# Kernel optimization log

Hardware: AMD Instinct MI355X
Metric: run time of the kernel (lower is better)

The kernel has to match this reference:

```python
import math
import jax, jax.numpy as jnp
import numpy as np


def setup_inputs() -> dict:
    key = jax.random.key(0)
    k1, k2 = jax.random.split(key)
    B, Sq, Sk, H, Hkv, D = 2, 2048, 2048, 32, 8, 128
    q = jax.random.normal(k1, (B, Sq, H, D), dtype=jnp.float32)
    kv = jax.random.normal(k2, (B, Sk, 2, Hkv, D), dtype=jnp.float32)
    return {"q": q, "kv": kv}


def reference(q, kv):
    # q: [B, Sq, H, D]; kv: [B, Sk, 2, Hkv, D]
    H = q.shape[2]
    Hkv = kv.shape[3]
    if Hkv != H:
        # GQA: '... hkv d -> ... (hkv g) d' == repeat each kv head g times consecutively
        kv = jnp.repeat(kv, H // Hkv, axis=3)
    k = kv[:, :, 0]  # [B, Sk, H, D]
    v = kv[:, :, 1]  # [B, Sk, H, D]
    softmax_scale = 1.0 / math.sqrt(q.shape[-1])
    scores = jnp.einsum('bthd,bshd->bhts', q, k * softmax_scale)  # [B, H, Sq, Sk]
    attention = jax.nn.softmax(scores, axis=-1)
    # dropout p=0.0 -> identity
    output = jnp.einsum('bhts,bshd->bthd', attention, v)  # [B, Sq, H, D]
    return output
```

## Files before the change

### kernel.cpp

```cpp
#include <hip/hip_runtime.h>
#include <hip/hip_bf16.h>

typedef __attribute__((ext_vector_type(8))) short bf8_t;
typedef __attribute__((ext_vector_type(16))) float f32x16;

#ifndef __has_builtin
#define __has_builtin(x) 0
#endif
#if __has_builtin(__builtin_amdgcn_exp2f)
#define EXP2F(x) __builtin_amdgcn_exp2f(x)
#else
#define EXP2F(x) exp2f(x)
#endif

#define B_ 2
#define SQ_ 2048
#define SK_ 2048
#define H_ 32
#define HKV_ 8
#define D_ 128
#define KVSTRIDE (2 * HKV_ * D_)
#define QSTRIDE (H_ * D_)
#define NT (SK_ / 64)
#define SCLOG (0.08838834764831845f * 1.4426950408889634f)

__device__ __forceinline__ unsigned short f2bf(float f) {
  unsigned int u = __builtin_bit_cast(unsigned int, f);
  u += 0x7fffu + ((u >> 16) & 1u);
  return (unsigned short)(u >> 16);
}
__device__ __forceinline__ unsigned int pk2(float a, float b) {
  return (unsigned int)f2bf(a) | ((unsigned int)f2bf(b) << 16);
}

__global__ void __launch_bounds__(512, 2)
fattn2(const float* __restrict__ q, const float* __restrict__ kv,
       float* __restrict__ out) {
  __shared__ __align__(16) char lds[32768];
  char* Ksh = lds;
  char* Vsh = lds + 16384;

  const int tid = threadIdx.x;
  const int lane = tid & 63;
  const int w = tid >> 6;
  const int ql = lane & 31;
  const int hi = lane >> 5;

  const int bid = blockIdx.x;
  const int qt = bid & 7;
  const int h = (bid >> 3) & 31;
  const int b = bid >> 8;
  const int hkv = h >> 2;

  const float* qbase = q + ((size_t)b * SQ_ * H_ + h) * D_;
  const float* kbase = kv + ((size_t)b * SK_ * 2 * HKV_ + hkv) * D_;
  const float* vbase = kv + ((size_t)b * SK_ * 2 * HKV_ + HKV_ + hkv) * D_;

  const int qrow = qt * 256 + w * 32 + ql;
  const float* qp = qbase + (size_t)qrow * QSTRIDE;
  bf8_t qf[8];
#pragma unroll
  for (int step = 0; step < 8; ++step) {
    const int d0 = step * 16 + hi * 8;
    float4 a = *(const float4*)(qp + d0);
    float4 c = *(const float4*)(qp + d0 + 4);
    bf8_t tq;
    tq[0] = (short)f2bf(a.x * SCLOG); tq[1] = (short)f2bf(a.y * SCLOG);
    tq[2] = (short)f2bf(a.z * SCLOG); tq[3] = (short)f2bf(a.w * SCLOG);
    tq[4] = (short)f2bf(c.x * SCLOG); tq[5] = (short)f2bf(c.y * SCLOG);
    tq[6] = (short)f2bf(c.z * SCLOG); tq[7] = (short)f2bf(c.w * SCLOG);
    qf[step] = tq;
  }

  const int vkv = lane;
  int kcol;
  {
    const int wv = vkv & 31, bb = vkv >> 5;
    const int T_ = (wv >> 2) & 1;
    const int rr = (wv & 3) + ((wv >> 3) << 2);
    kcol = (((bb << 1) + (rr >> 3)) << 4) + (T_ << 3) + (rr & 7);
  }

  f32x16 o[4];
  f32x16 st[2];
#pragma unroll
  for (int i = 0; i < 4; ++i)
#pragma unroll
    for (int r = 0; r < 16; ++r) o[i][r] = 0.f;
  float m = -INFINITY, l = 0.f;

  float4 krg[4], vrg[4];
  const int krow0 = tid >> 5;
  const int kc4 = tid & 31;
  auto load_tiles = [&](int T) {
    const float* kp0 = kbase + ((size_t)T * 64 + krow0) * KVSTRIDE + kc4 * 4;
#pragma unroll
    for (int i = 0; i < 4; ++i)
      krg[i] = *(const float4*)(kp0 + (size_t)(16 * i) * KVSTRIDE);
    const float* vp0 = vbase + ((size_t)T * 64 + vkv) * KVSTRIDE + w * 16;
#pragma unroll
    for (int i = 0; i < 4; ++i) vrg[i] = *(const float4*)(vp0 + 4 * i);
  };
  load_tiles(0);

  for (int t = 0; t < NT; ++t) {
    __syncthreads();

#pragma unroll
    for (int i = 0; i < 4; ++i) {
      const int row = krow0 + 16 * i;
      unsigned int off = (unsigned int)(row * 256 + kc4 * 8) ^
                         ((unsigned int)(row & 7) << 4);
      float4 kk = krg[i];
      unsigned long long pkw =
          (unsigned long long)f2bf(kk.x) |
          ((unsigned long long)f2bf(kk.y) << 16) |
          ((unsigned long long)f2bf(kk.z) << 32) |
          ((unsigned long long)f2bf(kk.w) << 48);
      *(unsigned long long*)(Ksh + off) = pkw;
    }
#pragma unroll
    for (int i = 0; i < 4; ++i) {
      float4 vv = vrg[i];
      float vals[4] = {vv.x, vv.y, vv.z, vv.w};
#pragma unroll
      for (int jj = 0; jj < 4; ++jj) {
        const int dj = w * 16 + i * 4 + jj;
        unsigned int off = (unsigned int)(dj * 128 + kcol * 2) ^
                           ((unsigned int)(dj & 7) << 4);
        *(unsigned short*)(Vsh + off) = f2bf(vals[jj]);
      }
    }
    __syncthreads();

    if (t + 1 < NT) load_tiles(t + 1);

#pragma unroll
    for (int r = 0; r < 16; ++r) { st[0][r] = 0.f; st[1][r] = 0.f; }
#pragma unroll
    for (int step = 0; step < 8; ++step) {
#pragma unroll
      for (int bb2 = 0; bb2 < 2; ++bb2) {
        const int row = bb2 * 32 + ql;
        unsigned int off = (unsigned int)(row * 256 + (step * 16 + hi * 8) * 2) ^
                           ((unsigned int)(row & 7) << 4);
        bf8_t kf = *(const bf8_t*)(Ksh + off);
        st[bb2] = __builtin_amdgcn_mfma_f32_32x32x16_bf16(kf, qf[step], st[bb2], 0, 0, 0);
      }
    }

    float mx = st[0][0];
#pragma unroll
    for (int r = 1; r < 16; ++r) mx = fmaxf(mx, st[0][r]);
#pragma unroll
    for (int r = 0; r < 16; ++r) mx = fmaxf(mx, st[1][r]);
    mx = fmaxf(mx, __shfl_xor(mx, 32));

    const int sk = __all(mx <= m + 8.0f);
    float mn, corr;
    if (sk) { mn = m; corr = 1.f; }
    else { mn = fmaxf(m, mx); corr = EXP2F(m - mn); m = mn; }

    float ls = 0.f;
#pragma unroll
    for (int bb2 = 0; bb2 < 2; ++bb2)
#pragma unroll
      for (int r = 0; r < 16; ++r) {
        float pv = EXP2F(st[bb2][r] - mn);
        st[bb2][r] = pv;
        ls += pv;
      }
    ls += __shfl_xor(ls, 32);
    l = l * corr + ls;
    if (!sk) {
#pragma unroll
      for (int i = 0; i < 4; ++i)
#pragma unroll
        for (int r = 0; r < 16; ++r) o[i][r] *= corr;
    }

#pragma unroll
    for (int ks = 0; ks < 4; ++ks) {
      const int b_ = ks >> 1, rb = (ks & 1) * 8;
      union { unsigned int u[4]; bf8_t v; } pw;
      pw.u[0] = pk2(st[b_][rb + 0], st[b_][rb + 1]);
      pw.u[1] = pk2(st[b_][rb + 2], st[b_][rb + 3]);
      pw.u[2] = pk2(st[b_][rb + 4], st[b_][rb + 5]);
      pw.u[3] = pk2(st[b_][rb + 6], st[b_][rb + 7]);
      const bf8_t pf = pw.v;
#pragma unroll
      for (int dblk = 0; dblk < 4; ++dblk) {
        const int d = dblk * 32 + ql;
        unsigned int off = (unsigned int)(d * 128 + (ks * 16 + hi * 8) * 2) ^
                           ((unsigned int)(d & 7) << 4);
        bf8_t vf = *(const bf8_t*)(Vsh + off);
        o[dblk] = __builtin_amdgcn_mfma_f32_32x32x16_bf16(vf, pf, o[dblk], 0, 0, 0);
      }
    }
  }

  __syncthreads();
  const float invl = 1.f / l;
  float* ep = (float*)(lds + (w << 12));
#pragma unroll
  for (int dblk = 0; dblk < 4; ++dblk) {
#pragma unroll
    for (int r = 0; r < 16; ++r) {
      const int dd = (r & 3) + 8 * (r >> 2) + 4 * hi;
      ep[dd * 32 + (ql ^ dd)] = o[dblk][r] * invl;
    }
#pragma unroll
    for (int p = 0; p < 16; ++p) {
      const int idx = p * 64 + lane;
      const int q2 = idx >> 5, dd2 = idx & 31;
      float v = ep[dd2 * 32 + (q2 ^ dd2)];
      out[((size_t)(b * SQ_ + qt * 256 + w * 32 + q2) * H_ + h) * D_ +
          dblk * 32 + dd2] = v;
    }
  }
}

extern "C" void kernel_launch(void* const* d_in, const int* in_sizes, int n_in,
                              void* d_out, int out_size, void* d_ws, size_t ws_size,
                              hipStream_t stream) {
  (void)in_sizes; (void)n_in; (void)out_size; (void)d_ws; (void)ws_size;
  const float* q = (const float*)d_in[0];
  const float* kv = (const float*)d_in[1];
  float* out = (float*)d_out;
  dim3 grid(B_ * H_ * 8);
  dim3 block(512);
  hipLaunchKernelGGL(fattn2, grid, block, 0, stream, q, kv, out);
}
```

Baseline: 342.2 us.

## Double-buffer K/V tiles in LDS and overlap staging with MFMA compute

Allocates two 32KB LDS buffers so the next K/V tile is converted and stored while the current tile is consumed. This leaves one barrier per iteration, and global loads are issued two tiles ahead. It also swaps manual bf16 rounding for packed hardware conversion, changes the V layout so each thread writes packed pairs, widens the swizzle, and raises wave priority around the MFMA blocks. Launch bounds drop to one block per CU because of the doubled LDS, which may cost occupancy and latency hiding.

```diff
diff --git a/kernel.cpp b/kernel.cpp
--- a/kernel.cpp
+++ b/kernel.cpp
@@ -22,23 +22,18 @@
 #define KVSTRIDE (2 * HKV_ * D_)
 #define QSTRIDE (H_ * D_)
 #define NT (SK_ / 64)
-#define SCLOG (0.08838834764831845f * 1.4426950408889634f)
-
-__device__ __forceinline__ unsigned short f2bf(float f) {
-  unsigned int u = __builtin_bit_cast(unsigned int, f);
-  u += 0x7fffu + ((u >> 16) & 1u);
-  return (unsigned short)(u >> 16);
+#define SCLOG 0.12754984679800714f
+
+__device__ __forceinline__ unsigned int cvtpk(float a, float b) {
+  union { __hip_bfloat162 h; unsigned int u; } c;
+  c.h = __float22bfloat162_rn(make_float2(a, b));
+  return c.u;
 }
-__device__ __forceinline__ unsigned int pk2(float a, float b) {
-  return (unsigned int)f2bf(a) | ((unsigned int)f2bf(b) << 16);
-}
-
-__global__ void __launch_bounds__(512, 2)
-fattn2(const float* __restrict__ q, const float* __restrict__ kv,
+
+__global__ void __launch_bounds__(512, 1)
+fattn3(const float* __restrict__ q, const float* __restrict__ kv,
        float* __restrict__ out) {
-  __shared__ __align__(16) char lds[32768];
-  char* Ksh = lds;
-  char* Vsh = lds + 16384;
+  __shared__ __align__(16) char lds[65536];
 
   const int tid = threadIdx.x;
   const int lane = tid & 63;
@@ -60,26 +55,69 @@
   const float* qp = qbase + (size_t)qrow * QSTRIDE;
   bf8_t qf[8];
 #pragma unroll
-  for (int step = 0; step < 8; ++step) {
-    const int d0 = step * 16 + hi * 8;
+  for (int s = 0; s < 8; ++s) {
+    const int d0 = s * 16 + hi * 8;
     float4 a = *(const float4*)(qp + d0);
     float4 c = *(const float4*)(qp + d0 + 4);
-    bf8_t tq;
-    tq[0] = (short)f2bf(a.x * SCLOG); tq[1] = (short)f2bf(a.y * SCLOG);
-    tq[2] = (short)f2bf(a.z * SCLOG); tq[3] = (short)f2bf(a.w * SCLOG);
-    tq[4] = (short)f2bf(c.x * SCLOG); tq[5] = (short)f2bf(c.y * SCLOG);
-    tq[6] = (short)f2bf(c.z * SCLOG); tq[7] = (short)f2bf(c.w * SCLOG);
-    qf[step] = tq;
-  }
-
-  const int vkv = lane;
-  int kcol;
+    union { unsigned int u[4]; bf8_t v; } t_;
+    t_.u[0] = cvtpk(a.x * SCLOG, a.y * SCLOG);
+    t_.u[1] = cvtpk(a.z * SCLOG, a.w * SCLOG);
+    t_.u[2] = cvtpk(c.x * SCLOG, c.y * SCLOG);
+    t_.u[3] = cvtpk(c.z * SCLOG, c.w * SCLOG);
+    qf[s] = t_.v;
+  }
+
+  const int krow = tid >> 5;
+  const int kc4 = tid & 31;
+  const int p = tid & 31;
+  const int dchunk = tid >> 5;
+  int kcol2;
   {
+    const int vkv = 2 * p;
     const int wv = vkv & 31, bb = vkv >> 5;
     const int T_ = (wv >> 2) & 1;
     const int rr = (wv & 3) + ((wv >> 3) << 2);
-    kcol = (((bb << 1) + (rr >> 3)) << 4) + (T_ << 3) + (rr & 7);
-  }
+    kcol2 = (((bb << 1) + (rr >> 3)) << 4) + (T_ << 3) + (rr & 7);
+  }
+
+  float4 krg[4], vrg[4];
+  auto load_tiles = [&](int T) {
+    const float* kp0 = kbase + ((size_t)T * 64 + krow) * KVSTRIDE + kc4 * 4;
+#pragma unroll
+    for (int i = 0; i < 4; ++i)
+      krg[i] = *(const float4*)(kp0 + (size_t)(16 * i) * KVSTRIDE);
+    const float* vp0 = vbase + ((size_t)T * 64 + 2 * p) * KVSTRIDE + dchunk * 8;
+    vrg[0] = *(const float4*)(vp0);
+    vrg[1] = *(const float4*)(vp0 + 4);
+    vrg[2] = *(const float4*)(vp0 + KVSTRIDE);
+    vrg[3] = *(const float4*)(vp0 + KVSTRIDE + 4);
+  };
+
+  auto store_tiles = [&](char* Ksh, char* Vsh) {
+#pragma unroll
+    for (int i = 0; i < 4; ++i) {
+      const int row = krow + 16 * i;
+      unsigned int off = ((unsigned int)(row * 256 + kc4 * 8)) ^
+                         ((unsigned int)(row & 15) << 4);
+      union { unsigned int u[2]; unsigned long long ll; } t_;
+      t_.u[0] = cvtpk(krg[i].x, krg[i].y);
+      t_.u[1] = cvtpk(krg[i].z, krg[i].w);
+      *(unsigned long long*)(Ksh + off) = t_.ll;
+    }
+    const float va[8] = {vrg[0].x, vrg[0].y, vrg[0].z, vrg[0].w,
+                         vrg[1].x, vrg[1].y, vrg[1].z, vrg[1].w};
+    const float vb[8] = {vrg[2].x, vrg[2].y, vrg[2].z, vrg[2].w,
+                         vrg[3].x, vrg[3].y, vrg[3].z, vrg[3].w};
+#pragma unroll
+    for (int jj = 0; jj < 8; ++jj) {
+      const int d = dchunk * 8 + jj;
+      const int r = d & 63;
+      unsigned int off =
+          ((unsigned int)(r * 256 + (d >> 6) * 128 + kcol2 * 2)) ^
+          ((unsigned int)(r & 15) << 4);
+      *(unsigned int*)(Vsh + off) = cvtpk(va[jj], vb[jj]);
+    }
+  };
 
   f32x16 o[4];
   f32x16 st[2];
@@ -89,71 +127,39 @@
     for (int r = 0; r < 16; ++r) o[i][r] = 0.f;
   float m = -INFINITY, l = 0.f;
 
-  float4 krg[4], vrg[4];
-  const int krow0 = tid >> 5;
-  const int kc4 = tid & 31;
-  auto load_tiles = [&](int T) {
-    const float* kp0 = kbase + ((size_t)T * 64 + krow0) * KVSTRIDE + kc4 * 4;
-#pragma unroll
-    for (int i = 0; i < 4; ++i)
-      krg[i] = *(const float4*)(kp0 + (size_t)(16 * i) * KVSTRIDE);
-    const float* vp0 = vbase + ((size_t)T * 64 + vkv) * KVSTRIDE + w * 16;
-#pragma unroll
-    for (int i = 0; i < 4; ++i) vrg[i] = *(const float4*)(vp0 + 4 * i);
-  };
   load_tiles(0);
+  store_tiles(lds, lds + 16384);
+  load_tiles(1);
+  __syncthreads();
 
   for (int t = 0; t < NT; ++t) {
-    __syncthreads();
-
-#pragma unroll
-    for (int i = 0; i < 4; ++i) {
-      const int row = krow0 + 16 * i;
-      unsigned int off = (unsigned int)(row * 256 + kc4 * 8) ^
-                         ((unsigned int)(row & 7) << 4);
-      float4 kk = krg[i];
-      unsigned long long pkw =
-          (unsigned long long)f2bf(kk.x) |
-          ((unsigned long long)f2bf(kk.y) << 16) |
-          ((unsigned long long)f2bf(kk.z) << 32) |
-          ((unsigned long long)f2bf(kk.w) << 48);
-      *(unsigned long long*)(Ksh + off) = pkw;
-    }
-#pragma unroll
-    for (int i = 0; i < 4; ++i) {
-      float4 vv = vrg[i];
-      float vals[4] = {vv.x, vv.y, vv.z, vv.w};
-#pragma unroll
-      for (int jj = 0; jj < 4; ++jj) {
-        const int dj = w * 16 + i * 4 + jj;
-        unsigned int off = (unsigned int)(dj * 128 + kcol * 2) ^
-                           ((unsigned int)(dj & 7) << 4);
-        *(unsigned short*)(Vsh + off) = f2bf(vals[jj]);
-      }
-    }
-    __syncthreads();
-
-    if (t + 1 < NT) load_tiles(t + 1);
+    char* Kc = lds + ((t & 1) << 15);
+    char* Vc = Kc + 16384;
 
 #pragma unroll
     for (int r = 0; r < 16; ++r) { st[0][r] = 0.f; st[1][r] = 0.f; }
-#pragma unroll
-    for (int step = 0; step < 8; ++step) {
+    __builtin_amdgcn_s_setprio(1);
+#pragma unroll
+    for (int s = 0; s < 8; ++s) {
 #pragma unroll
       for (int bb2 = 0; bb2 < 2; ++bb2) {
         const int row = bb2 * 32 + ql;
-        unsigned int off = (unsigned int)(row * 256 + (step * 16 + hi * 8) * 2) ^
-                           ((unsigned int)(row & 7) << 4);
-        bf8_t kf = *(const bf8_t*)(Ksh + off);
-        st[bb2] = __builtin_amdgcn_mfma_f32_32x32x16_bf16(kf, qf[step], st[bb2], 0, 0, 0);
+        unsigned int off = ((unsigned int)(row * 256 + s * 32 + hi * 16)) ^
+                           ((unsigned int)(row & 15) << 4);
+        bf8_t kf = *(const bf8_t*)(Kc + off);
+        st[bb2] =
+            __builtin_amdgcn_mfma_f32_32x32x16_bf16(kf, qf[s], st[bb2], 0, 0, 0);
       }
     }
-
-    float mx = st[0][0];
-#pragma unroll
-    for (int r = 1; r < 16; ++r) mx = fmaxf(mx, st[0][r]);
-#pragma unroll
-    for (int r = 0; r < 16; ++r) mx = fmaxf(mx, st[1][r]);
+    __builtin_amdgcn_s_setprio(0);
+
+    float mv[8];
+#pragma unroll
+    for (int r = 0; r < 8; ++r)
+      mv[r] = fmaxf(fmaxf(st[0][r], st[0][r + 8]),
+                    fmaxf(st[1][r], st[1][r + 8]));
+    float mx = fmaxf(fmaxf(fmaxf(mv[0], mv[1]), fmaxf(mv[2], mv[3])),
+                     fmaxf(fmaxf(mv[4], mv[5]), fmaxf(mv[6], mv[7])));
     mx = fmaxf(mx, __shfl_xor(mx, 32));
 
     const int sk = __all(mx <= m + 8.0f);
@@ -179,27 +185,38 @@
         for (int r = 0; r < 16; ++r) o[i][r] *= corr;
     }
 
+    if (t + 1 < NT) {
+      char* Kn = lds + (((t + 1) & 1) << 15);
+      store_tiles(Kn, Kn + 16384);
+      if (t + 2 < NT) load_tiles(t + 2);
+    }
+
+    __builtin_amdgcn_s_setprio(1);
 #pragma unroll
     for (int ks = 0; ks < 4; ++ks) {
       const int b_ = ks >> 1, rb = (ks & 1) * 8;
       union { unsigned int u[4]; bf8_t v; } pw;
-      pw.u[0] = pk2(st[b_][rb + 0], st[b_][rb + 1]);
-      pw.u[1] = pk2(st[b_][rb + 2], st[b_][rb + 3]);
-      pw.u[2] = pk2(st[b_][rb + 4], st[b_][rb + 5]);
-      pw.u[3] = pk2(st[b_][rb + 6], st[b_][rb + 7]);
+      pw.u[0] = cvtpk(st[b_][rb + 0], st[b_][rb + 1]);
+      pw.u[1] = cvtpk(st[b_][rb + 2], st[b_][rb + 3]);
+      pw.u[2] = cvtpk(st[b_][rb + 4], st[b_][rb + 5]);
+      pw.u[3] = cvtpk(st[b_][rb + 6], st[b_][rb + 7]);
       const bf8_t pf = pw.v;
 #pragma unroll
       for (int dblk = 0; dblk < 4; ++dblk) {
         const int d = dblk * 32 + ql;
-        unsigned int off = (unsigned int)(d * 128 + (ks * 16 + hi * 8) * 2) ^
-                           ((unsigned int)(d & 7) << 4);
-        bf8_t vf = *(const bf8_t*)(Vsh + off);
+        const int r = d & 63;
+        unsigned int off =
+            ((unsigned int)(r * 256 + (d >> 6) * 128 + ks * 32 + hi * 16)) ^
+            ((unsigned int)(r & 15) << 4);
+        bf8_t vf = *(const bf8_t*)(Vc + off);
         o[dblk] = __builtin_amdgcn_mfma_f32_32x32x16_bf16(vf, pf, o[dblk], 0, 0, 0);
       }
     }
-  }
-
-  __syncthreads();
+    __builtin_amdgcn_s_setprio(0);
+
+    __syncthreads();
+  }
+
   const float invl = 1.f / l;
   float* ep = (float*)(lds + (w << 12));
 #pragma unroll
@@ -210,8 +227,8 @@
       ep[dd * 32 + (ql ^ dd)] = o[dblk][r] * invl;
     }
 #pragma unroll
-    for (int p = 0; p < 16; ++p) {
-      const int idx = p * 64 + lane;
+    for (int pp = 0; pp < 16; ++pp) {
+      const int idx = pp * 64 + lane;
       const int q2 = idx >> 5, dd2 = idx & 31;
       float v = ep[dd2 * 32 + (q2 ^ dd2)];
       out[((size_t)(b * SQ_ + qt * 256 + w * 32 + q2) * H_ + h) * D_ +
@@ -229,5 +246,5 @@
   float* out = (float*)d_out;
   dim3 grid(B_ * H_ * 8);
   dim3 block(512);
-  hipLaunchKernelGGL(fattn2, grid, block, 0, stream, q, kv, out);
+  hipLaunchKernelGGL(fattn3, grid, block, 0, stream, q, kv, out);
 }
```

Result: faster. 289.1 us (-15.5%).
